# Performance work log

Measured on AMD Instinct MI355X. Metric: run time of the kernel, lower is better.

The kernel has to match this reference:

```python
import jax, jax.numpy as jnp
import numpy as np

B, T, C, H = 2, 2048, 1024, 16
D = C // H  # head dim = 64


def setup_inputs() -> dict:
    key = jax.random.key(0)
    ks = jax.random.split(key, 5)
    s_in = 1.0 / np.sqrt(C)
    return {
        "x": jax.random.normal(ks[0], (B, T, C), dtype=jnp.float32),
        "W_qkv": jax.random.uniform(ks[1], (C, 3 * C), jnp.float32, -s_in, s_in),
        "b_qkv": jax.random.uniform(ks[2], (3 * C,), jnp.float32, -s_in, s_in),
        "W_proj": jax.random.uniform(ks[3], (C, C), jnp.float32, -s_in, s_in),
        "b_proj": jax.random.uniform(ks[4], (C,), jnp.float32, -s_in, s_in),
    }


def reference(x, W_qkv, b_qkv, W_proj, b_proj):
    Bx, Tx, Cx = x.shape
    qkv = x @ W_qkv + b_qkv                      # [B,T,3C]
    q, k, v = jnp.split(qkv, 3, axis=2)          # each [B,T,C]
    # [B,T,C] -> [B,H,T,D]
    q = q.reshape(Bx, Tx, H, D).transpose(0, 2, 1, 3)
    k = k.reshape(Bx, Tx, H, D).transpose(0, 2, 1, 3)
    v = v.reshape(Bx, Tx, H, D).transpose(0, 2, 1, 3)
    scale = 1.0 / jnp.sqrt(jnp.asarray(D, dtype=x.dtype))
    scores = jnp.einsum("bhqd,bhkd->bhqk", q, k) * scale  # [B,H,T,T]
    causal = jnp.tril(jnp.ones((Tx, Tx), dtype=bool))
    scores = jnp.where(causal, scores, jnp.finfo(x.dtype).min)
    attn = jax.nn.softmax(scores, axis=-1)
    y = jnp.einsum("bhqk,bhkd->bhqd", attn, v)   # [B,H,T,D]
    y = y.transpose(0, 2, 1, 3).reshape(Bx, Tx, Cx)
    return y @ W_proj + b_proj
```

## Files before the change

kernel.cpp:

```cpp
#include <hip/hip_runtime.h>
#include <hip/hip_bf16.h>

#define Bb 2
#define Tt 2048
#define Cc 1024
#define Hh 16
#define Dd 64

typedef __bf16 bf16x8 __attribute__((ext_vector_type(8)));
typedef __bf16 bf16x4 __attribute__((ext_vector_type(4)));
typedef float f32x4 __attribute__((ext_vector_type(4)));

#define MFMA16(a, b, c) __builtin_amdgcn_mfma_f32_16x16x32_bf16((a), (b), (c), 0, 0, 0)

__device__ __forceinline__ bf16x8 ldg8(const __hip_bfloat16* p) {
  return *reinterpret_cast<const bf16x8*>(p);
}
__device__ __forceinline__ bf16x8 lds8(const __bf16* p) {
  return *reinterpret_cast<const bf16x8*>(p);
}

__device__ __forceinline__ void load_lds16(const __hip_bfloat16* g, __hip_bfloat16* l) {
  __builtin_amdgcn_global_load_lds(
      (const __attribute__((address_space(1))) void*)g,
      (__attribute__((address_space(3))) void*)l, 16, 0, 0);
}

__global__ __launch_bounds__(256) void cvt_f32_bf16(
    const float* __restrict__ in, __hip_bfloat16* __restrict__ out, int n) {
  const int i = (blockIdx.x * 256 + threadIdx.x) * 4;
  if (i + 3 < n) {
    const float4 v = *reinterpret_cast<const float4*>(in + i);
    out[i + 0] = __float2bfloat16(v.x);
    out[i + 1] = __float2bfloat16(v.y);
    out[i + 2] = __float2bfloat16(v.z);
    out[i + 3] = __float2bfloat16(v.w);
  }
}

__global__ __launch_bounds__(256) void transpose_cvt(
    const float* __restrict__ in, __hip_bfloat16* __restrict__ out,
    int R, int Cn) {
  __shared__ float tile[32][33];
  const int c0 = blockIdx.x * 32, r0 = blockIdx.y * 32;
  const int tx = threadIdx.x, ty = threadIdx.y;
#pragma unroll
  for (int i = 0; i < 32; i += 8)
    tile[ty + i][tx] = in[(size_t)(r0 + ty + i) * Cn + c0 + tx];
  __syncthreads();
#pragma unroll
  for (int i = 0; i < 32; i += 8)
    out[(size_t)(c0 + ty + i) * R + r0 + tx] = __float2bfloat16(tile[tx][ty + i]);
}

__global__ __launch_bounds__(256) void qkv_gemm(
    const __hip_bfloat16* __restrict__ x, const __hip_bfloat16* __restrict__ WT,
    const float* __restrict__ bias,
    __hip_bfloat16* __restrict__ Q, __hip_bfloat16* __restrict__ Kd,
    __hip_bfloat16* __restrict__ VT) {
  __shared__ __hip_bfloat16 As[128 * 32];
  __shared__ __hip_bfloat16 Bs[128 * 32];
  const int tid = threadIdx.x;
  const int wave = tid >> 6, lane = tid & 63;
  const int l16 = lane & 15, quad = lane >> 4;
  const int m0 = blockIdx.y * 128, n0 = blockIdx.x * 128;
  const int wm = (wave >> 1) * 64, wn = (wave & 1) * 64;

  const int srow = wave * 32 + (lane >> 2);
  const int kseg = (lane & 3) * 8;

  f32x4 acc[4][4] = {};

  for (int k0 = 0; k0 < Cc; k0 += 32) {
    __syncthreads();
#pragma unroll
    for (int j = 0; j < 2; ++j) {
      load_lds16(x + (size_t)(m0 + srow + j * 16) * Cc + k0 + kseg,
                 As + (wave * 32 + j * 16) * 32);
      load_lds16(WT + (size_t)(n0 + srow + j * 16) * Cc + k0 + kseg,
                 Bs + (wave * 32 + j * 16) * 32);
    }
    __syncthreads();

    bf16x8 af[4], bfr[4];
#pragma unroll
    for (int i = 0; i < 4; ++i) {
      af[i] = ldg8(As + (wm + i * 16 + l16) * 32 + quad * 8);
      bfr[i] = ldg8(Bs + (wn + i * 16 + l16) * 32 + quad * 8);
    }
#pragma unroll
    for (int i = 0; i < 4; ++i)
#pragma unroll
      for (int jn = 0; jn < 4; ++jn)
        acc[i][jn] = MFMA16(af[i], bfr[jn], acc[i][jn]);
  }

  const int sect = n0 >> 10;
#pragma unroll
  for (int jn = 0; jn < 4; ++jn) {
    const int n = n0 + wn + jn * 16 + l16;
    const float bv = bias[n];
    const int ch = n & 1023;
    const int h = ch >> 6, d = ch & 63;
#pragma unroll
    for (int i = 0; i < 4; ++i) {
#pragma unroll
      for (int r = 0; r < 4; ++r) {
        const int m = m0 + wm + i * 16 + quad * 4 + r;
        const int b = m >> 11, t = m & 2047;
        const __hip_bfloat16 o = __float2bfloat16(acc[i][jn][r] + bv);
        const int bh = b * Hh + h;
        if (sect == 0)      Q[((size_t)bh * Tt + t) * Dd + d] = o;
        else if (sect == 1) Kd[((size_t)bh * Tt + t) * Dd + d] = o;
        else                VT[((size_t)bh * Dd + d) * Tt + t] = o;
      }
    }
  }
}

__global__ __launch_bounds__(256) void attn(
    const __hip_bfloat16* __restrict__ Q, const __hip_bfloat16* __restrict__ K,
    const __hip_bfloat16* __restrict__ VT, __hip_bfloat16* __restrict__ O) {
  const int tid = threadIdx.x;
  const int wave = tid >> 6, lane = tid & 63;
  const int l16 = lane & 15, quad = lane >> 4;
  const int bh = blockIdx.z * Hh + blockIdx.y;

  const __hip_bfloat16* Qh = Q + (size_t)bh * Tt * Dd;
  const __hip_bfloat16* Kh = K + (size_t)bh * Tt * Dd;
  const __hip_bfloat16* Vh = VT + (size_t)bh * Dd * Tt;
  __hip_bfloat16* Oh = O + (size_t)bh * Tt * Dd;

  __shared__ __align__(16) __bf16 Kt[64 * 72];
  __shared__ __align__(16) __bf16 Vt[64 * 72];
  __shared__ __align__(16) __bf16 Pt[4][16 * 72];

  const float SC = 0.18033688011112042f;
  const int skey = tid >> 3;
  const int sd = (tid & 7) * 8;

  for (int phase = 0; phase < 2; ++phase) {
    const int qb = phase ? (Tt / 64 - 1) - blockIdx.x : blockIdx.x;
    const int q0 = qb * 64;
    const int qrow = q0 + wave * 16 + l16;

    const bf16x8 qf0 = ldg8(Qh + (size_t)qrow * Dd + quad * 8);
    const bf16x8 qf1 = ldg8(Qh + (size_t)qrow * Dd + 32 + quad * 8);

    f32x4 o_acc[4] = {};
    float m_s = -INFINITY, l_s = 0.f;

    const int nk = qb + 1;
    bf16x8 ka = ldg8(Kh + (size_t)skey * Dd + sd);
    bf16x8 kb = ldg8(Kh + (size_t)(32 + skey) * Dd + sd);
    bf16x8 va = ldg8(Vh + (size_t)skey * Tt + sd);
    bf16x8 vb = ldg8(Vh + (size_t)(32 + skey) * Tt + sd);

    for (int kt0 = 0; kt0 < nk; ++kt0) {
      const int k0 = kt0 * 64;
      __syncthreads();
      *reinterpret_cast<bf16x8*>(&Kt[skey * 72 + sd]) = ka;
      *reinterpret_cast<bf16x8*>(&Kt[(32 + skey) * 72 + sd]) = kb;
      *reinterpret_cast<bf16x8*>(&Vt[skey * 72 + sd]) = va;
      *reinterpret_cast<bf16x8*>(&Vt[(32 + skey) * 72 + sd]) = vb;
      if (kt0 + 1 < nk) {
        const int k1 = k0 + 64;
        ka = ldg8(Kh + (size_t)(k1 + skey) * Dd + sd);
        kb = ldg8(Kh + (size_t)(k1 + 32 + skey) * Dd + sd);
        va = ldg8(Vh + (size_t)skey * Tt + k1 + sd);
        vb = ldg8(Vh + (size_t)(32 + skey) * Tt + k1 + sd);
      }
      __syncthreads();

      f32x4 st[4];
#pragma unroll
      for (int kt = 0; kt < 4; ++kt) {
        const __bf16* kr = &Kt[(kt * 16 + l16) * 72 + quad * 8];
        f32x4 z = {};
        z = MFMA16(lds8(kr), qf0, z);
        st[kt] = MFMA16(lds8(kr + 32), qf1, z);
      }

      float v[16];
      float mx = -INFINITY;
#pragma unroll
      for (int kt = 0; kt < 4; ++kt)
#pragma unroll
        for (int r = 0; r < 4; ++r) {
          const int key = k0 + kt * 16 + quad * 4 + r;
          const float val = (key <= qrow) ? st[kt][r] * SC : -INFINITY;
          v[kt * 4 + r] = val;
          mx = fmaxf(mx, val);
        }
      mx = fmaxf(mx, __shfl_xor(mx, 16, 64));
      mx = fmaxf(mx, __shfl_xor(mx, 32, 64));
      const float mnew = fmaxf(m_s, mx);
      const float alpha = exp2f(m_s - mnew);
      m_s = mnew;

      float rs = 0.f;
#pragma unroll
      for (int kt = 0; kt < 4; ++kt) {
        bf16x4 pk;
#pragma unroll
        for (int r = 0; r < 4; ++r) {
          const float p = exp2f(v[kt * 4 + r] - mnew);
          rs += p;
          pk[r] = (__bf16)p;
        }
        *reinterpret_cast<bf16x4*>(&Pt[wave][l16 * 72 + kt * 16 + quad * 4]) = pk;
      }
      rs += __shfl_xor(rs, 16, 64);
      rs += __shfl_xor(rs, 32, 64);
      l_s = l_s * alpha + rs;

#pragma unroll
      for (int dt = 0; dt < 4; ++dt) o_acc[dt] *= alpha;

      const bf16x8 pf0 = lds8(&Pt[wave][l16 * 72 + quad * 8]);
      const bf16x8 pf1 = lds8(&Pt[wave][l16 * 72 + 32 + quad * 8]);
#pragma unroll
      for (int dt = 0; dt < 4; ++dt) {
        const __bf16* vr = &Vt[(dt * 16 + l16) * 72];
        o_acc[dt] = MFMA16(lds8(vr + quad * 8), pf0, o_acc[dt]);
        o_acc[dt] = MFMA16(lds8(vr + 32 + quad * 8), pf1, o_acc[dt]);
      }
    }

    const float inv = 1.f / l_s;
#pragma unroll
    for (int dt = 0; dt < 4; ++dt) {
      bf16x4 ov;
#pragma unroll
      for (int r = 0; r < 4; ++r) ov[r] = (__bf16)(o_acc[dt][r] * inv);
      *reinterpret_cast<bf16x4*>(&Oh[(size_t)qrow * Dd + dt * 16 + quad * 4]) = ov;
    }
  }
}

__global__ __launch_bounds__(256) void proj_gemm(
    const __hip_bfloat16* __restrict__ O, const __hip_bfloat16* __restrict__ WT,
    const float* __restrict__ bias, float* __restrict__ out) {
  __shared__ __hip_bfloat16 As[128 * 32];
  __shared__ __hip_bfloat16 Bs[128 * 32];
  const int tid = threadIdx.x;
  const int wave = tid >> 6, lane = tid & 63;
  const int l16 = lane & 15, quad = lane >> 4;
  const int m0 = blockIdx.y * 128, n0 = blockIdx.x * 128;
  const int wm = (wave >> 1) * 64, wn = (wave & 1) * 64;

  const int srow = wave * 32 + (lane >> 2);
  const int kseg = (lane & 3) * 8;

  f32x4 acc[4][4] = {};

  for (int k0 = 0; k0 < Cc; k0 += 32) {
    const int k = k0 + kseg;
    const int h = k >> 6, d = k & 63;
    __syncthreads();
#pragma unroll
    for (int j = 0; j < 2; ++j) {
      const int m = m0 + srow + j * 16;
      const int b = m >> 11, t = m & 2047;
      load_lds16(O + ((size_t)(b * Hh + h) * Tt + t) * Dd + d,
                 As + (wave * 32 + j * 16) * 32);
      load_lds16(WT + (size_t)(n0 + srow + j * 16) * Cc + k0 + kseg,
                 Bs + (wave * 32 + j * 16) * 32);
    }
    __syncthreads();

    bf16x8 af[4], bfr[4];
#pragma unroll
    for (int i = 0; i < 4; ++i) {
      af[i] = ldg8(As + (wm + i * 16 + l16) * 32 + quad * 8);
      bfr[i] = ldg8(Bs + (wn + i * 16 + l16) * 32 + quad * 8);
    }
#pragma unroll
    for (int i = 0; i < 4; ++i)
#pragma unroll
      for (int jn = 0; jn < 4; ++jn)
        acc[i][jn] = MFMA16(af[i], bfr[jn], acc[i][jn]);
  }

#pragma unroll
  for (int jn = 0; jn < 4; ++jn) {
    const int n = n0 + wn + jn * 16 + l16;
    const float bv = bias[n];
#pragma unroll
    for (int i = 0; i < 4; ++i)
#pragma unroll
      for (int r = 0; r < 4; ++r) {
        const int m = m0 + wm + i * 16 + quad * 4 + r;
        out[(size_t)m * Cc + n] = acc[i][jn][r] + bv;
      }
  }
}

extern "C" void kernel_launch(void* const* d_in, const int* in_sizes, int n_in,
                              void* d_out, int out_size, void* d_ws, size_t ws_size,
                              hipStream_t stream) {
  const float* x      = (const float*)d_in[0];
  const float* W_qkv  = (const float*)d_in[1];
  const float* b_qkv  = (const float*)d_in[2];
  const float* W_proj = (const float*)d_in[3];
  const float* b_proj = (const float*)d_in[4];
  float* out = (float*)d_out;

  __hip_bfloat16* ws = (__hip_bfloat16*)d_ws;
  const size_t NBHTD = (size_t)Bb * Hh * Tt * Dd;
  __hip_bfloat16* Qw  = ws;
  __hip_bfloat16* Kw  = ws + NBHTD;
  __hip_bfloat16* VTw = ws + 2 * NBHTD;
  __hip_bfloat16* Ow  = ws + 3 * NBHTD;
  __hip_bfloat16* xb  = ws + 4 * NBHTD;
  __hip_bfloat16* WTqkv  = xb + NBHTD;
  __hip_bfloat16* WTproj = WTqkv + (size_t)3 * Cc * Cc;

  cvt_f32_bf16<<<dim3(4096), dim3(256), 0, stream>>>(x, xb, Bb * Tt * Cc);
  transpose_cvt<<<dim3(96, 32), dim3(32, 8), 0, stream>>>(W_qkv, WTqkv, Cc, 3 * Cc);
  transpose_cvt<<<dim3(32, 32), dim3(32, 8), 0, stream>>>(W_proj, WTproj, Cc, Cc);
  qkv_gemm<<<dim3(24, 32), 256, 0, stream>>>(xb, WTqkv, b_qkv, Qw, Kw, VTw);
  attn<<<dim3(Tt / 128, Hh, Bb), 256, 0, stream>>>(Qw, Kw, VTw, Ow);
  proj_gemm<<<dim3(8, 32), 256, 0, stream>>>(Ow, WTproj, b_proj, out);
}
```

Measured before the change: 207.8 us.

## Process paired query blocks in one KV sweep to share K/V tile loads

The attention kernel used to run two sequential phases, one for query block i and one for its mirror block, each reloading K/V tiles. It now streams K/V once over the longer causal range and applies each staged tile to both query blocks, with the short block skipping tiles past its diagonal. Causal masking is also limited to the diagonal tile, so off-diagonal tiles skip the compare and select. This removes about a third of the K/V global loads and barriers, at the cost of more registers for two accumulator sets, which may lower occupancy.

```diff
diff --git a/kernel.cpp b/kernel.cpp
--- a/kernel.cpp
+++ b/kernel.cpp
@@ -136,53 +136,41 @@
   __shared__ __align__(16) __bf16 Pt[4][16 * 72];
 
   const float SC = 0.18033688011112042f;
-  const int skey = tid >> 3;
-  const int sd = (tid & 7) * 8;
-
-  for (int phase = 0; phase < 2; ++phase) {
-    const int qb = phase ? (Tt / 64 - 1) - blockIdx.x : blockIdx.x;
-    const int q0 = qb * 64;
-    const int qrow = q0 + wave * 16 + l16;
-
-    const bf16x8 qf0 = ldg8(Qh + (size_t)qrow * Dd + quad * 8);
-    const bf16x8 qf1 = ldg8(Qh + (size_t)qrow * Dd + 32 + quad * 8);
-
-    f32x4 o_acc[4] = {};
-    float m_s = -INFINITY, l_s = 0.f;
-
-    const int nk = qb + 1;
-    bf16x8 ka = ldg8(Kh + (size_t)skey * Dd + sd);
-    bf16x8 kb = ldg8(Kh + (size_t)(32 + skey) * Dd + sd);
-    bf16x8 va = ldg8(Vh + (size_t)skey * Tt + sd);
-    bf16x8 vb = ldg8(Vh + (size_t)(32 + skey) * Tt + sd);
-
-    for (int kt0 = 0; kt0 < nk; ++kt0) {
-      const int k0 = kt0 * 64;
-      __syncthreads();
-      *reinterpret_cast<bf16x8*>(&Kt[skey * 72 + sd]) = ka;
-      *reinterpret_cast<bf16x8*>(&Kt[(32 + skey) * 72 + sd]) = kb;
-      *reinterpret_cast<bf16x8*>(&Vt[skey * 72 + sd]) = va;
-      *reinterpret_cast<bf16x8*>(&Vt[(32 + skey) * 72 + sd]) = vb;
-      if (kt0 + 1 < nk) {
-        const int k1 = k0 + 64;
-        ka = ldg8(Kh + (size_t)(k1 + skey) * Dd + sd);
-        kb = ldg8(Kh + (size_t)(k1 + 32 + skey) * Dd + sd);
-        va = ldg8(Vh + (size_t)skey * Tt + k1 + sd);
-        vb = ldg8(Vh + (size_t)(32 + skey) * Tt + k1 + sd);
-      }
-      __syncthreads();
-
-      f32x4 st[4];
-#pragma unroll
-      for (int kt = 0; kt < 4; ++kt) {
-        const __bf16* kr = &Kt[(kt * 16 + l16) * 72 + quad * 8];
-        f32x4 z = {};
-        z = MFMA16(lds8(kr), qf0, z);
-        st[kt] = MFMA16(lds8(kr + 32), qf1, z);
-      }
-
-      float v[16];
-      float mx = -INFINITY;
+  const int skey = tid >> 3, sd = (tid & 7) * 8;
+
+  const int qbA = blockIdx.x;
+  const int qbB = (Tt / 64 - 1) - qbA;
+  const int qrowA = qbA * 64 + wave * 16 + l16;
+  const int qrowB = qbB * 64 + wave * 16 + l16;
+
+  const bf16x8 qA0 = ldg8(Qh + (size_t)qrowA * Dd + quad * 8);
+  const bf16x8 qA1 = ldg8(Qh + (size_t)qrowA * Dd + 32 + quad * 8);
+  const bf16x8 qB0 = ldg8(Qh + (size_t)qrowB * Dd + quad * 8);
+  const bf16x8 qB1 = ldg8(Qh + (size_t)qrowB * Dd + 32 + quad * 8);
+
+  f32x4 oA[4] = {}, oB[4] = {};
+  float mA = -INFINITY, lA = 0.f, mB = -INFINITY, lB = 0.f;
+
+  const int nkB = qbB + 1;
+
+  bf16x8 ka = ldg8(Kh + (size_t)skey * Dd + sd);
+  bf16x8 kb = ldg8(Kh + (size_t)(32 + skey) * Dd + sd);
+  bf16x8 va = ldg8(Vh + (size_t)skey * Tt + sd);
+  bf16x8 vb = ldg8(Vh + (size_t)(32 + skey) * Tt + sd);
+
+  auto process = [&](const bf16x8& q0f, const bf16x8& q1f, f32x4* oacc,
+                     float& m_s, float& l_s, int qrow, int k0, bool diag) {
+    f32x4 st[4];
+#pragma unroll
+    for (int kt = 0; kt < 4; ++kt) {
+      const __bf16* kr = &Kt[(kt * 16 + l16) * 72 + quad * 8];
+      f32x4 z = {};
+      z = MFMA16(lds8(kr), q0f, z);
+      st[kt] = MFMA16(lds8(kr + 32), q1f, z);
+    }
+    float v[16];
+    float mx = -INFINITY;
+    if (diag) {
 #pragma unroll
       for (int kt = 0; kt < 4; ++kt)
 #pragma unroll
@@ -192,49 +180,79 @@
           v[kt * 4 + r] = val;
           mx = fmaxf(mx, val);
         }
-      mx = fmaxf(mx, __shfl_xor(mx, 16, 64));
-      mx = fmaxf(mx, __shfl_xor(mx, 32, 64));
-      const float mnew = fmaxf(m_s, mx);
-      const float alpha = exp2f(m_s - mnew);
-      m_s = mnew;
-
-      float rs = 0.f;
-#pragma unroll
-      for (int kt = 0; kt < 4; ++kt) {
-        bf16x4 pk;
+    } else {
+#pragma unroll
+      for (int kt = 0; kt < 4; ++kt)
 #pragma unroll
         for (int r = 0; r < 4; ++r) {
-          const float p = exp2f(v[kt * 4 + r] - mnew);
-          rs += p;
-          pk[r] = (__bf16)p;
+          const float val = st[kt][r] * SC;
+          v[kt * 4 + r] = val;
+          mx = fmaxf(mx, val);
         }
-        *reinterpret_cast<bf16x4*>(&Pt[wave][l16 * 72 + kt * 16 + quad * 4]) = pk;
+    }
+    mx = fmaxf(mx, __shfl_xor(mx, 16, 64));
+    mx = fmaxf(mx, __shfl_xor(mx, 32, 64));
+    const float mnew = fmaxf(m_s, mx);
+    const float alpha = exp2f(m_s - mnew);
+    m_s = mnew;
+    float rs = 0.f;
+#pragma unroll
+    for (int kt = 0; kt < 4; ++kt) {
+      bf16x4 pk;
+#pragma unroll
+      for (int r = 0; r < 4; ++r) {
+        const float p = exp2f(v[kt * 4 + r] - mnew);
+        rs += p;
+        pk[r] = (__bf16)p;
       }
-      rs += __shfl_xor(rs, 16, 64);
-      rs += __shfl_xor(rs, 32, 64);
-      l_s = l_s * alpha + rs;
-
-#pragma unroll
-      for (int dt = 0; dt < 4; ++dt) o_acc[dt] *= alpha;
-
-      const bf16x8 pf0 = lds8(&Pt[wave][l16 * 72 + quad * 8]);
-      const bf16x8 pf1 = lds8(&Pt[wave][l16 * 72 + 32 + quad * 8]);
-#pragma unroll
-      for (int dt = 0; dt < 4; ++dt) {
-        const __bf16* vr = &Vt[(dt * 16 + l16) * 72];
-        o_acc[dt] = MFMA16(lds8(vr + quad * 8), pf0, o_acc[dt]);
-        o_acc[dt] = MFMA16(lds8(vr + 32 + quad * 8), pf1, o_acc[dt]);
-      }
-    }
-
-    const float inv = 1.f / l_s;
+      *reinterpret_cast<bf16x4*>(&Pt[wave][l16 * 72 + kt * 16 + quad * 4]) = pk;
+    }
+    rs += __shfl_xor(rs, 16, 64);
+    rs += __shfl_xor(rs, 32, 64);
+    l_s = l_s * alpha + rs;
+#pragma unroll
+    for (int dt = 0; dt < 4; ++dt) oacc[dt] *= alpha;
+    const bf16x8 pf0 = lds8(&Pt[wave][l16 * 72 + quad * 8]);
+    const bf16x8 pf1 = lds8(&Pt[wave][l16 * 72 + 32 + quad * 8]);
 #pragma unroll
     for (int dt = 0; dt < 4; ++dt) {
-      bf16x4 ov;
-#pragma unroll
-      for (int r = 0; r < 4; ++r) ov[r] = (__bf16)(o_acc[dt][r] * inv);
-      *reinterpret_cast<bf16x4*>(&Oh[(size_t)qrow * Dd + dt * 16 + quad * 4]) = ov;
-    }
+      const __bf16* vr = &Vt[(dt * 16 + l16) * 72];
+      oacc[dt] = MFMA16(lds8(vr + quad * 8), pf0, oacc[dt]);
+      oacc[dt] = MFMA16(lds8(vr + 32 + quad * 8), pf1, oacc[dt]);
+    }
+  };
+
+  for (int kt0 = 0; kt0 < nkB; ++kt0) {
+    const int k0 = kt0 * 64;
+    __syncthreads();
+    *reinterpret_cast<bf16x8*>(&Kt[skey * 72 + sd]) = ka;
+    *reinterpret_cast<bf16x8*>(&Kt[(32 + skey) * 72 + sd]) = kb;
+    *reinterpret_cast<bf16x8*>(&Vt[skey * 72 + sd]) = va;
+    *reinterpret_cast<bf16x8*>(&Vt[(32 + skey) * 72 + sd]) = vb;
+    if (kt0 + 1 < nkB) {
+      const int k1 = k0 + 64;
+      ka = ldg8(Kh + (size_t)(k1 + skey) * Dd + sd);
+      kb = ldg8(Kh + (size_t)(k1 + 32 + skey) * Dd + sd);
+      va = ldg8(Vh + (size_t)skey * Tt + k1 + sd);
+      vb = ldg8(Vh + (size_t)(32 + skey) * Tt + k1 + sd);
+    }
+    __syncthreads();
+
+    process(qB0, qB1, oB, mB, lB, qrowB, k0, kt0 == qbB);
+    if (kt0 <= qbA) process(qA0, qA1, oA, mA, lA, qrowA, k0, kt0 == qbA);
+  }
+
+  const float invA = 1.f / lA, invB = 1.f / lB;
+#pragma unroll
+  for (int dt = 0; dt < 4; ++dt) {
+    bf16x4 ovA, ovB;
+#pragma unroll
+    for (int r = 0; r < 4; ++r) {
+      ovA[r] = (__bf16)(oA[dt][r] * invA);
+      ovB[r] = (__bf16)(oB[dt][r] * invB);
+    }
+    *reinterpret_cast<bf16x4*>(&Oh[(size_t)qrowA * Dd + dt * 16 + quad * 4]) = ovA;
+    *reinterpret_cast<bf16x4*>(&Oh[(size_t)qrowB * Dd + dt * 16 + quad * 4]) = ovB;
   }
 }
 
```

New measurement: 202.0 us. 2.8% less time.
